# Kernel optimization log

Measured on AMD Instinct MI355X. Metric: run time of the kernel, lower is better.

## Reference

```python
import jax, jax.numpy as jnp
import numpy as np

EPS = 1e-5

def headwise_linear(x, w):
    # x: [B,S,D], w: [NH, DH_out, DH_in] block-diagonal linear per head
    B, S, D = x.shape
    NH, O, DH = w.shape
    xh = x.reshape(B, S, NH, DH)
    return jnp.einsum('bshd,hod->bsho', xh, w).reshape(B, S, NH * O)

def setup_inputs() -> dict:
    key = jax.random.key(0)
    ks = jax.random.split(key, 10)
    B, S, D, NH, K = 8, 4096, 768, 4, 4
    DH = D // NH
    small = (2.0 / (5.0 * D)) ** 0.5  # small_init scale
    return {
        'x': jax.random.normal(ks[0], (B, S, D), jnp.float32),
        'conv_w': jax.random.normal(ks[1], (D, 1, K), jnp.float32) * (1.0 / K ** 0.5),
        'conv_b': jnp.zeros((D,), jnp.float32),
        'w_f': jax.random.normal(ks[2], (NH, DH, DH), jnp.float32) * small,
        'w_i': jax.random.normal(ks[3], (NH, DH, DH), jnp.float32) * small,
        'w_z': jax.random.normal(ks[4], (NH, DH, DH), jnp.float32) * small,
        'w_o': jax.random.normal(ks[5], (NH, DH, DH), jnp.float32) * small,
        'r_kernel': jax.random.normal(ks[6], (NH, DH, 4, DH), jnp.float32) * (1.0 / DH ** 0.5),
        'r_bias': jnp.zeros((4, NH, DH), jnp.float32),
        'gn_weight': jnp.ones((D,), jnp.float32),
    }

def reference(x, conv_w, conv_b, w_f, w_i, w_z, w_o, r_kernel, r_bias, gn_weight):
    B, S, D = x.shape
    NH, DH = r_kernel.shape[0], r_kernel.shape[1]
    K = conv_w.shape[-1]
    # --- causal depthwise conv1d + SiLU ---
    xt = jnp.transpose(x, (0, 2, 1))  # [B,D,S]
    xc = jax.lax.conv_general_dilated(xt, conv_w, (1,), [(K - 1, 0)],
                                      feature_group_count=D)
    x_conv = jax.nn.silu(jnp.transpose(xc + conv_b[None, :, None], (0, 2, 1)))
    # --- headwise gate projections (note: original code feeds fgate->i, igate->f) ---
    gi = headwise_linear(x_conv, w_f)
    gf = headwise_linear(x_conv, w_i)
    gz = headwise_linear(x, w_z)
    go = headwise_linear(x, w_o)
    Wx = jnp.stack([gi, gf, gz, go], axis=2).reshape(B, S, 4, NH, DH)
    Wx = jnp.transpose(Wx, (1, 0, 2, 3, 4))  # [S,B,4,NH,DH]
    # --- sLSTM recurrent scan with exponential gating + stabilizer m ---
    def step(carry, wx_t):
        y, c, n, m = carry  # each [B,NH,DH]
        Ry = jnp.einsum('bhd,hdge->bghe', y, r_kernel)  # [B,4,NH,DH]
        raw = wx_t + Ry + r_bias[None]
        iraw, fraw, zraw, oraw = raw[:, 0], raw[:, 1], raw[:, 2], raw[:, 3]
        logfplusm = m + jax.nn.log_sigmoid(fraw)
        mnew = jnp.maximum(iraw, logfplusm)
        igate = jnp.exp(iraw - mnew)
        fgate = jnp.exp(logfplusm - mnew)
        cnew = fgate * c + igate * jnp.tanh(zraw)
        nnew = fgate * n + igate
        ynew = jax.nn.sigmoid(oraw) * cnew / nnew
        return (ynew, cnew, nnew, mnew), ynew
    init = tuple(jnp.zeros((B, NH, DH), x.dtype) for _ in range(4))
    _, ys = jax.lax.scan(step, init, Wx)  # [S,B,NH,DH]
    y = jnp.transpose(ys, (1, 2, 0, 3))  # [B,NH,S,DH]
    # --- multi-head layer norm (group norm with NH groups over DH) ---
    mean = y.mean(-1, keepdims=True)
    var = y.var(-1, keepdims=True)
    yn = (y - mean) * jax.lax.rsqrt(var + EPS)
    yn = yn * gn_weight.reshape(1, NH, 1, DH)
    return jnp.transpose(yn, (0, 2, 1, 3)).reshape(B, S, NH * DH)
```

## Files before the change

### kernel.cpp

```cpp
#include <hip/hip_runtime.h>
#include <hip/hip_bf16.h>
#include <math.h>

#define B_ 8
#define S_ 4096
#define D_ 768
#define NH_ 4
#define DH_ 192
#define NTOT_ 768

typedef __attribute__((ext_vector_type(8))) short short8;
typedef __attribute__((ext_vector_type(4))) float floatx4;
typedef __attribute__((ext_vector_type(4))) short short4v;
typedef __attribute__((ext_vector_type(4))) unsigned int uint4v;
typedef _Float16 f16;

__device__ __forceinline__ short f2bs(float f) {
  union { float f; unsigned u; } v; v.f = f;
  unsigned r = v.u + 0x7FFFu + ((v.u >> 16) & 1u);
  return (short)(r >> 16);
}
__device__ __forceinline__ float bs2f(unsigned short s) {
  union { unsigned u; float f; } v; v.u = ((unsigned)s) << 16;
  return v.f;
}
__device__ __forceinline__ unsigned packh2(float lo, float hi) {
  union { f16 h[2]; unsigned u; } x;
  x.h[0] = (f16)lo; x.h[1] = (f16)hi;
  return x.u;
}

__device__ __forceinline__ float DOT2(unsigned r, unsigned y, float acc) {
  asm("v_dot2_f32_f16 %0, %1, %2, %0" : "+v"(acc) : "v"(r), "v"(y));
  return acc;
}

template<int CTRL>
__device__ __forceinline__ float qperm(float x) {
  return __int_as_float(__builtin_amdgcn_mov_dpp(__float_as_int(x), CTRL, 0xf, 0xf, true));
}

__global__ __launch_bounds__(256) void wconv_kernel(
    const float* __restrict__ wf, const float* __restrict__ wi,
    const float* __restrict__ wz, const float* __restrict__ wo,
    short* __restrict__ Wbf)
{
  int idx = blockIdx.x * 256 + threadIdx.x;
  int hg = idx / (DH_ * DH_);
  int r  = idx % (DH_ * DH_);
  int h = hg >> 2, g = hg & 3;
  const float* W = (g == 0) ? wf : (g == 1) ? wi : (g == 2) ? wz : wo;
  Wbf[idx] = f2bs(W[(size_t)h * DH_ * DH_ + r]);
}

__global__ __launch_bounds__(256) void conv_silu_kernel(
    const float* __restrict__ x, const float* __restrict__ cw, const float* __restrict__ cb,
    short* __restrict__ xb, short* __restrict__ xcb)
{
  const int b  = blockIdx.x / (S_ / 64);
  const int s0 = (blockIdx.x % (S_ / 64)) * 64;
  const int tid = threadIdx.x;
  float wv[3][4], bias[3], win[3][3];
  for (int j = 0; j < 3; ++j) {
    int d = tid + j * 256;
    for (int k = 0; k < 4; ++k) wv[j][k] = cw[d * 4 + k];
    bias[j] = cb[d];
    for (int p = 0; p < 3; ++p) {
      int s = s0 - 3 + p;
      win[j][p] = (s >= 0) ? x[((size_t)b * S_ + s) * D_ + d] : 0.f;
    }
  }
  for (int i = 0; i < 64; ++i) {
    size_t base = ((size_t)b * S_ + (s0 + i)) * D_;
    for (int j = 0; j < 3; ++j) {
      int d = tid + j * 256;
      float xc = x[base + d];
      float a = bias[j] + win[j][0] * wv[j][0] + win[j][1] * wv[j][1]
                        + win[j][2] * wv[j][2] + xc * wv[j][3];
      float sv = a / (1.f + __expf(-a));
      xb[base + d]  = f2bs(xc);
      xcb[base + d] = f2bs(sv);
      win[j][0] = win[j][1]; win[j][1] = win[j][2]; win[j][2] = xc;
    }
  }
}

__global__ __launch_bounds__(256) void proj_kernel(
    const short* __restrict__ xb, const short* __restrict__ xcb,
    const short* __restrict__ Wbf, const float* __restrict__ rb,
    short* __restrict__ P)
{
  const int hg = blockIdx.y;
  const int h = hg >> 2, g = hg & 3;
  const short* A  = (g < 2) ? xcb : xb;
  const short* Wb = Wbf + (size_t)hg * (DH_ * DH_);
  const int tid = threadIdx.x, w = tid >> 6, l = tid & 63;
  const int l15 = l & 15, lg = l >> 4;
  const int R0 = blockIdx.x * 256 + w * 64;

  float rbv[12];
#pragma unroll
  for (int nt = 0; nt < 12; ++nt)
    rbv[nt] = rb[(g * NH_ + h) * DH_ + l15 + nt * 16];

  for (int mp = 0; mp < 2; ++mp) {
    const int rb0 = R0 + mp * 32;
    floatx4 acc[2][12];
    for (int u = 0; u < 2; ++u)
      for (int nt = 0; nt < 12; ++nt) acc[u][nt] = (floatx4){0.f, 0.f, 0.f, 0.f};
    const short* Ar = A + (size_t)(rb0 + l15) * D_ + h * DH_ + lg * 8;
    const short* Bp = Wb + l15 * DH_ + lg * 8;
    for (int kk = 0; kk < 6; ++kk) {
      short8 a0 = *(const short8*)(Ar + kk * 32);
      short8 a1 = *(const short8*)(Ar + (size_t)16 * D_ + kk * 32);
      for (int nt = 0; nt < 12; ++nt) {
        short8 bf = *(const short8*)(Bp + nt * 16 * DH_ + kk * 32);
        acc[0][nt] = __builtin_amdgcn_mfma_f32_16x16x32_bf16(a0, bf, acc[0][nt], 0, 0, 0);
        acc[1][nt] = __builtin_amdgcn_mfma_f32_16x16x32_bf16(a1, bf, acc[1][nt], 0, 0, 0);
      }
    }
    for (int u = 0; u < 2; ++u) {
      for (int q = 0; q < 4; ++q) {
        int row = rb0 + u * 16 + lg * 4 + q;
        int s = row & (S_ - 1);
        int bb = row >> 12;
        size_t ob = (((size_t)h * B_ + bb) * S_ + s) * NTOT_ + l15 * 4 + g;
        for (int nt = 0; nt < 12; ++nt)
          P[ob + nt * 64] = f2bs(acc[u][nt][q] + rbv[nt]);
      }
    }
  }
}

__global__ __launch_bounds__(768)
void scan_kernel(short* P_, const float* __restrict__ rk)
{
  const int bid = blockIdx.x;
  const int h = bid >> 3;
  const int t0 = threadIdx.x;
  const int e = t0 >> 2, q = t0 & 3;
  const int w = t0 >> 6, l = t0 & 63;
  const int l15 = l & 15, lg = l >> 4;

  __shared__ __align__(16) f16 y_f16[DH_];
  __shared__ __align__(16) unsigned short y_bf[DH_];
  __shared__ __align__(16) float raw_lds[3][DH_];

  const float* Rh = rk + (size_t)h * (DH_ * NTOT_);

  unsigned Ri[24];
#pragma unroll
  for (int j = 0; j < 24; ++j) {
    const int k0 = 48 * q + 2 * j;
    Ri[j] = packh2(Rh[(size_t)k0 * NTOT_ + e], Rh[(size_t)(k0 + 1) * NTOT_ + e]);
  }

  short8 Bf[3][6];
#pragma unroll
  for (int gg = 0; gg < 3; ++gg) {
#pragma unroll
    for (int kk = 0; kk < 6; ++kk) {
      short8 v;
#pragma unroll
      for (int j = 0; j < 8; ++j) {
        const int k = kk * 32 + lg * 8 + j;
        v[j] = f2bs(Rh[(size_t)k * NTOT_ + (gg + 1) * DH_ + w * 16 + l15]);
      }
      Bf[gg][kk] = v;
    }
  }

  if (t0 < DH_) { y_f16[t0] = (f16)0.f; y_bf[t0] = 0; }

  float c = 0.f, nrm = 0.f, m = 0.f;
  short* Pc = P_ + (size_t)bid * S_ * NTOT_;
  short4v wxc = *(const short4v*)(Pc + e * 4);
  __syncthreads();

#pragma unroll 1
  for (int t = 0; t < S_; ++t) {
    short4v wxn = {};
    if (t + 1 < S_) wxn = *(const short4v*)(Pc + (size_t)(t + 1) * NTOT_ + e * 4);

    floatx4 acc0 = (floatx4){0.f,0.f,0.f,0.f};
    floatx4 acc1 = (floatx4){0.f,0.f,0.f,0.f};
    floatx4 acc2 = (floatx4){0.f,0.f,0.f,0.f};
    float a0 = 0.f;
#pragma unroll
    for (int kk = 0; kk < 6; ++kk) {
      short8 A = *(const short8*)((const short*)y_bf + kk * 32 + lg * 8);
      acc0 = __builtin_amdgcn_mfma_f32_16x16x32_bf16(A, Bf[0][kk], acc0, 0, 0, 0);
      acc1 = __builtin_amdgcn_mfma_f32_16x16x32_bf16(A, Bf[1][kk], acc1, 0, 0, 0);
      acc2 = __builtin_amdgcn_mfma_f32_16x16x32_bf16(A, Bf[2][kk], acc2, 0, 0, 0);
      uint4v Y = *(const uint4v*)((const f16*)y_f16 + q * 48 + kk * 8);
      a0 = DOT2(Ri[kk * 4 + 0], Y[0], a0);
      a0 = DOT2(Ri[kk * 4 + 1], Y[1], a0);
      a0 = DOT2(Ri[kk * 4 + 2], Y[2], a0);
      a0 = DOT2(Ri[kk * 4 + 3], Y[3], a0);
    }
    a0 += qperm<0xB1>(a0);  a0 += qperm<0x4E>(a0);
    if (l < 16) {
      raw_lds[0][w * 16 + l] = acc0[0];
      raw_lds[1][w * 16 + l] = acc1[0];
      raw_lds[2][w * 16 + l] = acc2[0];
    }
    __syncthreads();

    float ir  = bs2f((unsigned short)wxc[0]) + a0;
    float fr  = bs2f((unsigned short)wxc[1]) + raw_lds[0][e];
    float zr  = bs2f((unsigned short)wxc[2]) + raw_lds[1][e];
    float orr = bs2f((unsigned short)wxc[3]) + raw_lds[2][e];

    float lsf = fminf(fr, 0.f) - __logf(1.f + __expf(-fabsf(fr)));
    float lfm = m + lsf;
    float mnew = fmaxf(ir, lfm);
    float ig = __expf(ir - mnew);
    float fg = __expf(lfm - mnew);
    float e2z = __expf(2.f * zr);
    float tz = 1.f - 2.f * __builtin_amdgcn_rcpf(e2z + 1.f);
    c   = fg * c + ig * tz;
    nrm = fg * nrm + ig;
    m = mnew;
    float sg = __builtin_amdgcn_rcpf(1.f + __expf(-orr));
    float y = sg * c * __builtin_amdgcn_rcpf(nrm);

    if (q == 0) {
      f16 yh = (f16)y;
      y_f16[e] = yh;
      y_bf[e] = (unsigned short)f2bs(y);
      union { f16 hh; short ss; } uv; uv.hh = yh;
      Pc[(size_t)t * NTOT_ + e] = uv.ss;
    }
    wxc = wxn;
    __syncthreads();
  }
}

__global__ __launch_bounds__(256) void gnorm_kernel(
    const short* __restrict__ yws, const float* __restrict__ gnw,
    float* __restrict__ out)
{
  const int row = blockIdx.x * 4 + (threadIdx.x >> 6);
  const int l = threadIdx.x & 63;
  const int h = row >> 15;
  const int b = (row >> 12) & 7;
  const int s = row & (S_ - 1);
  const short* yr = yws + (size_t)row * NTOT_;
  float v[3];
  float su = 0.f, sq = 0.f;
#pragma unroll
  for (int j = 0; j < 3; ++j) {
    unsigned short u = (unsigned short)yr[l + j * 64];
    union { unsigned short u; f16 h; } cv; cv.u = u;
    v[j] = (float)cv.h;
    su += v[j]; sq += v[j] * v[j];
  }
  for (int off = 32; off; off >>= 1) {
    su += __shfl_xor(su, off);
    sq += __shfl_xor(sq, off);
  }
  float mean = su * (1.f / DH_);
  float var = sq * (1.f / DH_) - mean * mean;
  float rs = rsqrtf(var + 1e-5f);
  float* orow = out + ((size_t)b * S_ + s) * D_ + h * DH_;
#pragma unroll
  for (int j = 0; j < 3; ++j)
    orow[l + j * 64] = (v[j] - mean) * rs * gnw[h * DH_ + l + j * 64];
}

extern "C" void kernel_launch(void* const* d_in, const int* in_sizes, int n_in,
                              void* d_out, int out_size, void* d_ws, size_t ws_size,
                              hipStream_t stream) {
  const float* x   = (const float*)d_in[0];
  const float* cw  = (const float*)d_in[1];
  const float* cb  = (const float*)d_in[2];
  const float* wf  = (const float*)d_in[3];
  const float* wi  = (const float*)d_in[4];
  const float* wz  = (const float*)d_in[5];
  const float* wo  = (const float*)d_in[6];
  const float* rk  = (const float*)d_in[7];
  const float* rb  = (const float*)d_in[8];
  const float* gnw = (const float*)d_in[9];
  float* out = (float*)d_out;

  short* P   = (short*)d_ws;
  short* Wbf = (short*)((char*)d_ws + (size_t)201326592);
  short* xb  = (short*)d_out;
  short* xcb = (short*)((char*)d_out + (size_t)50331648);

  wconv_kernel<<<dim3(2304), 256, 0, stream>>>(wf, wi, wz, wo, Wbf);
  conv_silu_kernel<<<dim3(512), 256, 0, stream>>>(x, cw, cb, xb, xcb);
  proj_kernel<<<dim3(128, 16), 256, 0, stream>>>(xb, xcb, Wbf, rb, P);
  scan_kernel<<<dim3(32), 768, 0, stream>>>(P, rk);
  gnorm_kernel<<<dim3(32768), 256, 0, stream>>>(P, gnw, out);
}
```

Baseline: 5.687 ms.

## Batch all eight sequences per head into one MFMA-based scan block

The recurrent scan now runs one workgroup per head instead of one per head and batch. The eight batch rows fill the MFMA M dimension, so all four gates come from f16 MFMAs and the separate dot2 path for the input gate is gone. Each thread updates two batch states per step, y is double-buffered in LDS, and the gate results move through a per-wave LDS exchange that needs no barrier. That leaves one block barrier per timestep instead of two, at the cost of more serial gate arithmetic per thread, only 4 active workgroups, and f16 instead of bf16 for the recurrent operand.

```diff
diff --git a/kernel.cpp b/kernel.cpp
--- a/kernel.cpp
+++ b/kernel.cpp
@@ -12,8 +12,8 @@
 typedef __attribute__((ext_vector_type(8))) short short8;
 typedef __attribute__((ext_vector_type(4))) float floatx4;
 typedef __attribute__((ext_vector_type(4))) short short4v;
-typedef __attribute__((ext_vector_type(4))) unsigned int uint4v;
 typedef _Float16 f16;
+typedef __attribute__((ext_vector_type(8))) _Float16 h8;
 
 __device__ __forceinline__ short f2bs(float f) {
   union { float f; unsigned u; } v; v.f = f;
@@ -23,21 +23,6 @@
 __device__ __forceinline__ float bs2f(unsigned short s) {
   union { unsigned u; float f; } v; v.u = ((unsigned)s) << 16;
   return v.f;
-}
-__device__ __forceinline__ unsigned packh2(float lo, float hi) {
-  union { f16 h[2]; unsigned u; } x;
-  x.h[0] = (f16)lo; x.h[1] = (f16)hi;
-  return x.u;
-}
-
-__device__ __forceinline__ float DOT2(unsigned r, unsigned y, float acc) {
-  asm("v_dot2_f32_f16 %0, %1, %2, %0" : "+v"(acc) : "v"(r), "v"(y));
-  return acc;
-}
-
-template<int CTRL>
-__device__ __forceinline__ float qperm(float x) {
-  return __int_as_float(__builtin_amdgcn_mov_dpp(__float_as_int(x), CTRL, 0xf, 0xf, true));
 }
 
 __global__ __launch_bounds__(256) void wconv_kernel(
@@ -135,103 +120,123 @@
 __global__ __launch_bounds__(768)
 void scan_kernel(short* P_, const float* __restrict__ rk)
 {
-  const int bid = blockIdx.x;
-  const int h = bid >> 3;
+  const int h  = blockIdx.x;
   const int t0 = threadIdx.x;
-  const int e = t0 >> 2, q = t0 & 3;
-  const int w = t0 >> 6, l = t0 & 63;
+  const int w  = t0 >> 6, l = t0 & 63;
   const int l15 = l & 15, lg = l >> 4;
 
-  __shared__ __align__(16) f16 y_f16[DH_];
-  __shared__ __align__(16) unsigned short y_bf[DH_];
-  __shared__ __align__(16) float raw_lds[3][DH_];
+  __shared__ __align__(16) f16 y_lds[2][16][200];
+  __shared__ __align__(16) float raw_lds[12][8][16][4];
 
   const float* Rh = rk + (size_t)h * (DH_ * NTOT_);
 
-  unsigned Ri[24];
-#pragma unroll
-  for (int j = 0; j < 24; ++j) {
-    const int k0 = 48 * q + 2 * j;
-    Ri[j] = packh2(Rh[(size_t)k0 * NTOT_ + e], Rh[(size_t)(k0 + 1) * NTOT_ + e]);
-  }
-
-  short8 Bf[3][6];
-#pragma unroll
-  for (int gg = 0; gg < 3; ++gg) {
+  h8 Bf[4][6];
+#pragma unroll
+  for (int g = 0; g < 4; ++g) {
 #pragma unroll
     for (int kk = 0; kk < 6; ++kk) {
-      short8 v;
+      h8 v;
 #pragma unroll
       for (int j = 0; j < 8; ++j) {
         const int k = kk * 32 + lg * 8 + j;
-        v[j] = f2bs(Rh[(size_t)k * NTOT_ + (gg + 1) * DH_ + w * 16 + l15]);
+        v[j] = (f16)Rh[(size_t)k * NTOT_ + g * DH_ + w * 16 + l15];
       }
-      Bf[gg][kk] = v;
-    }
-  }
-
-  if (t0 < DH_) { y_f16[t0] = (f16)0.f; y_bf[t0] = 0; }
-
-  float c = 0.f, nrm = 0.f, m = 0.f;
-  short* Pc = P_ + (size_t)bid * S_ * NTOT_;
-  short4v wxc = *(const short4v*)(Pc + e * 4);
+      Bf[g][kk] = v;
+    }
+  }
+
+  for (int idx = t0; idx < 2 * 16 * 200; idx += 768)
+    ((f16*)y_lds)[idx] = (f16)0.f;
+
+  const int e  = w * 16 + l15;
+  const int c0 = lg, c1 = lg + 4;
+  short* Pb0 = P_ + ((size_t)(h * B_ + c0) * S_) * NTOT_;
+  short* Pb1 = P_ + ((size_t)(h * B_ + c1) * S_) * NTOT_;
+
+  float cc0 = 0.f, nn0 = 0.f, mm0 = 0.f;
+  float cc1 = 0.f, nn1 = 0.f, mm1 = 0.f;
+  short4v wxc0 = *(const short4v*)(Pb0 + e * 4);
+  short4v wxc1 = *(const short4v*)(Pb1 + e * 4);
   __syncthreads();
 
 #pragma unroll 1
   for (int t = 0; t < S_; ++t) {
-    short4v wxn = {};
-    if (t + 1 < S_) wxn = *(const short4v*)(Pc + (size_t)(t + 1) * NTOT_ + e * 4);
-
-    floatx4 acc0 = (floatx4){0.f,0.f,0.f,0.f};
-    floatx4 acc1 = (floatx4){0.f,0.f,0.f,0.f};
-    floatx4 acc2 = (floatx4){0.f,0.f,0.f,0.f};
-    float a0 = 0.f;
+    short4v wxn0 = {}, wxn1 = {};
+    if (t + 1 < S_) {
+      wxn0 = *(const short4v*)(Pb0 + (size_t)(t + 1) * NTOT_ + e * 4);
+      wxn1 = *(const short4v*)(Pb1 + (size_t)(t + 1) * NTOT_ + e * 4);
+    }
+    const int cur = t & 1, nxt = cur ^ 1;
+
+    floatx4 a0 = (floatx4){0.f,0.f,0.f,0.f};
+    floatx4 a1 = (floatx4){0.f,0.f,0.f,0.f};
+    floatx4 a2 = (floatx4){0.f,0.f,0.f,0.f};
+    floatx4 a3 = (floatx4){0.f,0.f,0.f,0.f};
 #pragma unroll
     for (int kk = 0; kk < 6; ++kk) {
-      short8 A = *(const short8*)((const short*)y_bf + kk * 32 + lg * 8);
-      acc0 = __builtin_amdgcn_mfma_f32_16x16x32_bf16(A, Bf[0][kk], acc0, 0, 0, 0);
-      acc1 = __builtin_amdgcn_mfma_f32_16x16x32_bf16(A, Bf[1][kk], acc1, 0, 0, 0);
-      acc2 = __builtin_amdgcn_mfma_f32_16x16x32_bf16(A, Bf[2][kk], acc2, 0, 0, 0);
-      uint4v Y = *(const uint4v*)((const f16*)y_f16 + q * 48 + kk * 8);
-      a0 = DOT2(Ri[kk * 4 + 0], Y[0], a0);
-      a0 = DOT2(Ri[kk * 4 + 1], Y[1], a0);
-      a0 = DOT2(Ri[kk * 4 + 2], Y[2], a0);
-      a0 = DOT2(Ri[kk * 4 + 3], Y[3], a0);
-    }
-    a0 += qperm<0xB1>(a0);  a0 += qperm<0x4E>(a0);
-    if (l < 16) {
-      raw_lds[0][w * 16 + l] = acc0[0];
-      raw_lds[1][w * 16 + l] = acc1[0];
-      raw_lds[2][w * 16 + l] = acc2[0];
-    }
-    __syncthreads();
-
-    float ir  = bs2f((unsigned short)wxc[0]) + a0;
-    float fr  = bs2f((unsigned short)wxc[1]) + raw_lds[0][e];
-    float zr  = bs2f((unsigned short)wxc[2]) + raw_lds[1][e];
-    float orr = bs2f((unsigned short)wxc[3]) + raw_lds[2][e];
-
-    float lsf = fminf(fr, 0.f) - __logf(1.f + __expf(-fabsf(fr)));
-    float lfm = m + lsf;
-    float mnew = fmaxf(ir, lfm);
-    float ig = __expf(ir - mnew);
-    float fg = __expf(lfm - mnew);
-    float e2z = __expf(2.f * zr);
-    float tz = 1.f - 2.f * __builtin_amdgcn_rcpf(e2z + 1.f);
-    c   = fg * c + ig * tz;
-    nrm = fg * nrm + ig;
-    m = mnew;
-    float sg = __builtin_amdgcn_rcpf(1.f + __expf(-orr));
-    float y = sg * c * __builtin_amdgcn_rcpf(nrm);
-
-    if (q == 0) {
-      f16 yh = (f16)y;
-      y_f16[e] = yh;
-      y_bf[e] = (unsigned short)f2bs(y);
-      union { f16 hh; short ss; } uv; uv.hh = yh;
-      Pc[(size_t)t * NTOT_ + e] = uv.ss;
-    }
-    wxc = wxn;
+      h8 A = *(const h8*)&y_lds[cur][l15][kk * 32 + lg * 8];
+      a0 = __builtin_amdgcn_mfma_f32_16x16x32_f16(A, Bf[0][kk], a0, 0, 0, 0);
+      a1 = __builtin_amdgcn_mfma_f32_16x16x32_f16(A, Bf[1][kk], a1, 0, 0, 0);
+      a2 = __builtin_amdgcn_mfma_f32_16x16x32_f16(A, Bf[2][kk], a2, 0, 0, 0);
+      a3 = __builtin_amdgcn_mfma_f32_16x16x32_f16(A, Bf[3][kk], a3, 0, 0, 0);
+    }
+    if (l < 32) {
+#pragma unroll
+      for (int j = 0; j < 4; ++j) {
+        floatx4 v = (floatx4){a0[j], a1[j], a2[j], a3[j]};
+        *(floatx4*)&raw_lds[w][lg * 4 + j][l15][0] = v;
+      }
+    }
+    floatx4 r0 = *(const floatx4*)&raw_lds[w][c0][l15][0];
+    floatx4 r1 = *(const floatx4*)&raw_lds[w][c1][l15][0];
+
+    f16 yh0, yh1;
+    {
+      float ir  = bs2f((unsigned short)wxc0[0]) + r0[0];
+      float fr  = bs2f((unsigned short)wxc0[1]) + r0[1];
+      float zr  = bs2f((unsigned short)wxc0[2]) + r0[2];
+      float orr = bs2f((unsigned short)wxc0[3]) + r0[3];
+      float lsf = fminf(fr, 0.f) - __logf(1.f + __expf(-fabsf(fr)));
+      float lfm = mm0 + lsf;
+      float mnew = fmaxf(ir, lfm);
+      float ig = __expf(ir - mnew);
+      float fg = __expf(lfm - mnew);
+      float e2z = __expf(2.f * zr);
+      float tz = 1.f - 2.f * __builtin_amdgcn_rcpf(e2z + 1.f);
+      cc0 = fg * cc0 + ig * tz;
+      nn0 = fg * nn0 + ig;
+      mm0 = mnew;
+      float sg = __builtin_amdgcn_rcpf(1.f + __expf(-orr));
+      yh0 = (f16)(sg * cc0 * __builtin_amdgcn_rcpf(nn0));
+    }
+    {
+      float ir  = bs2f((unsigned short)wxc1[0]) + r1[0];
+      float fr  = bs2f((unsigned short)wxc1[1]) + r1[1];
+      float zr  = bs2f((unsigned short)wxc1[2]) + r1[2];
+      float orr = bs2f((unsigned short)wxc1[3]) + r1[3];
+      float lsf = fminf(fr, 0.f) - __logf(1.f + __expf(-fabsf(fr)));
+      float lfm = mm1 + lsf;
+      float mnew = fmaxf(ir, lfm);
+      float ig = __expf(ir - mnew);
+      float fg = __expf(lfm - mnew);
+      float e2z = __expf(2.f * zr);
+      float tz = 1.f - 2.f * __builtin_amdgcn_rcpf(e2z + 1.f);
+      cc1 = fg * cc1 + ig * tz;
+      nn1 = fg * nn1 + ig;
+      mm1 = mnew;
+      float sg = __builtin_amdgcn_rcpf(1.f + __expf(-orr));
+      yh1 = (f16)(sg * cc1 * __builtin_amdgcn_rcpf(nn1));
+    }
+
+    y_lds[nxt][c0][e] = yh0;
+    y_lds[nxt][c1][e] = yh1;
+    {
+      union { f16 hh; short ss; } u0, u1;
+      u0.hh = yh0; u1.hh = yh1;
+      Pb0[(size_t)t * NTOT_ + e] = u0.ss;
+      Pb1[(size_t)t * NTOT_ + e] = u1.ss;
+    }
+    wxc0 = wxn0; wxc1 = wxn1;
     __syncthreads();
   }
 }
@@ -291,6 +296,6 @@
   wconv_kernel<<<dim3(2304), 256, 0, stream>>>(wf, wi, wz, wo, Wbf);
   conv_silu_kernel<<<dim3(512), 256, 0, stream>>>(x, cw, cb, xb, xcb);
   proj_kernel<<<dim3(128, 16), 256, 0, stream>>>(xb, xcb, Wbf, rb, P);
-  scan_kernel<<<dim3(32), 768, 0, stream>>>(P, rk);
+  scan_kernel<<<dim3(4), 768, 0, stream>>>(P, rk);
   gnorm_kernel<<<dim3(32768), 256, 0, stream>>>(P, gnw, out);
 }
```

After: 5.426 ms. -4.6%, faster.

## Rebalance sLSTM recurrent gates between dot2 VALU and f16 MFMA tiles

Applied to the files above, without the earlier changes.

In the scan kernel, the forget gate's recurrent matvec moves from MFMA to per-thread v_dot2 accumulation, joining the input gate. Only the z and o gates stay on MFMA, with each wave now computing two 16-column tiles. This cuts the MFMA work per wave in the latency-bound per-timestep loop but adds VALU dot work. The MFMA path also switches from bf16 to f16, so a single y buffer feeds both paths and the bf16 conversion and store disappear. The y buffer in LDS is double-buffered by timestep parity.

```diff
diff --git a/kernel.cpp b/kernel.cpp
--- a/kernel.cpp
+++ b/kernel.cpp
@@ -14,6 +14,7 @@
 typedef __attribute__((ext_vector_type(4))) short short4v;
 typedef __attribute__((ext_vector_type(4))) unsigned int uint4v;
 typedef _Float16 f16;
+typedef __attribute__((ext_vector_type(8))) _Float16 h8;
 
 __device__ __forceinline__ short f2bs(float f) {
   union { float f; unsigned u; } v; v.f = f;
@@ -34,7 +35,6 @@
   asm("v_dot2_f32_f16 %0, %1, %2, %0" : "+v"(acc) : "v"(r), "v"(y));
   return acc;
 }
-
 template<int CTRL>
 __device__ __forceinline__ float qperm(float x) {
   return __int_as_float(__builtin_amdgcn_mov_dpp(__float_as_int(x), CTRL, 0xf, 0xf, true));
@@ -142,35 +142,40 @@
   const int w = t0 >> 6, l = t0 & 63;
   const int l15 = l & 15, lg = l >> 4;
 
-  __shared__ __align__(16) f16 y_f16[DH_];
-  __shared__ __align__(16) unsigned short y_bf[DH_];
-  __shared__ __align__(16) float raw_lds[3][DH_];
+  __shared__ __align__(16) f16 y_lds[2][256];
+  __shared__ __align__(16) float raw_lds[2][DH_];
 
   const float* Rh = rk + (size_t)h * (DH_ * NTOT_);
 
-  unsigned Ri[24];
+  unsigned Rr[2][24];
 #pragma unroll
   for (int j = 0; j < 24; ++j) {
     const int k0 = 48 * q + 2 * j;
-    Ri[j] = packh2(Rh[(size_t)k0 * NTOT_ + e], Rh[(size_t)(k0 + 1) * NTOT_ + e]);
-  }
-
-  short8 Bf[3][6];
-#pragma unroll
-  for (int gg = 0; gg < 3; ++gg) {
+    Rr[0][j] = packh2(Rh[(size_t)k0 * NTOT_ + e],
+                      Rh[(size_t)(k0 + 1) * NTOT_ + e]);
+    Rr[1][j] = packh2(Rh[(size_t)k0 * NTOT_ + DH_ + e],
+                      Rh[(size_t)(k0 + 1) * NTOT_ + DH_ + e]);
+  }
+
+  h8 Bf[2][6];
+#pragma unroll
+  for (int tt = 0; tt < 2; ++tt) {
+    const int tile = 2 * w + tt;
+    const int gate = 2 + (tile >= 12);
+    const int ecol = (tile % 12) * 16 + l15;
 #pragma unroll
     for (int kk = 0; kk < 6; ++kk) {
-      short8 v;
+      h8 v;
 #pragma unroll
       for (int j = 0; j < 8; ++j) {
         const int k = kk * 32 + lg * 8 + j;
-        v[j] = f2bs(Rh[(size_t)k * NTOT_ + (gg + 1) * DH_ + w * 16 + l15]);
+        v[j] = (f16)Rh[(size_t)k * NTOT_ + gate * DH_ + ecol];
       }
-      Bf[gg][kk] = v;
-    }
-  }
-
-  if (t0 < DH_) { y_f16[t0] = (f16)0.f; y_bf[t0] = 0; }
+      Bf[tt][kk] = v;
+    }
+  }
+
+  if (t0 < 512) ((f16*)y_lds)[t0] = (f16)0.f;
 
   float c = 0.f, nrm = 0.f, m = 0.f;
   short* Pc = P_ + (size_t)bid * S_ * NTOT_;
@@ -182,34 +187,43 @@
     short4v wxn = {};
     if (t + 1 < S_) wxn = *(const short4v*)(Pc + (size_t)(t + 1) * NTOT_ + e * 4);
 
+    const f16* ycur = y_lds[t & 1];
+
     floatx4 acc0 = (floatx4){0.f,0.f,0.f,0.f};
     floatx4 acc1 = (floatx4){0.f,0.f,0.f,0.f};
-    floatx4 acc2 = (floatx4){0.f,0.f,0.f,0.f};
-    float a0 = 0.f;
 #pragma unroll
     for (int kk = 0; kk < 6; ++kk) {
-      short8 A = *(const short8*)((const short*)y_bf + kk * 32 + lg * 8);
-      acc0 = __builtin_amdgcn_mfma_f32_16x16x32_bf16(A, Bf[0][kk], acc0, 0, 0, 0);
-      acc1 = __builtin_amdgcn_mfma_f32_16x16x32_bf16(A, Bf[1][kk], acc1, 0, 0, 0);
-      acc2 = __builtin_amdgcn_mfma_f32_16x16x32_bf16(A, Bf[2][kk], acc2, 0, 0, 0);
-      uint4v Y = *(const uint4v*)((const f16*)y_f16 + q * 48 + kk * 8);
-      a0 = DOT2(Ri[kk * 4 + 0], Y[0], a0);
-      a0 = DOT2(Ri[kk * 4 + 1], Y[1], a0);
-      a0 = DOT2(Ri[kk * 4 + 2], Y[2], a0);
-      a0 = DOT2(Ri[kk * 4 + 3], Y[3], a0);
+      h8 A = *(const h8*)&ycur[kk * 32 + lg * 8];
+      acc0 = __builtin_amdgcn_mfma_f32_16x16x32_f16(A, Bf[0][kk], acc0, 0, 0, 0);
+      acc1 = __builtin_amdgcn_mfma_f32_16x16x32_f16(A, Bf[1][kk], acc1, 0, 0, 0);
+    }
+
+    const f16* yb = ycur + q * 48;
+    float a0 = 0.f, a1 = 0.f;
+#pragma unroll
+    for (int i = 0; i < 6; ++i) {
+      uint4v Y = *(const uint4v*)(yb + i * 8);
+#pragma unroll
+      for (int u = 0; u < 4; ++u) {
+        const int j = i * 4 + u;
+        a0 = DOT2(Rr[0][j], Y[u], a0);
+        a1 = DOT2(Rr[1][j], Y[u], a1);
+      }
     }
     a0 += qperm<0xB1>(a0);  a0 += qperm<0x4E>(a0);
+    a1 += qperm<0xB1>(a1);  a1 += qperm<0x4E>(a1);
+
     if (l < 16) {
-      raw_lds[0][w * 16 + l] = acc0[0];
-      raw_lds[1][w * 16 + l] = acc1[0];
-      raw_lds[2][w * 16 + l] = acc2[0];
+      const int tile0 = 2 * w, tile1 = 2 * w + 1;
+      raw_lds[tile0 >= 12][(tile0 % 12) * 16 + l15] = acc0[0];
+      raw_lds[tile1 >= 12][(tile1 % 12) * 16 + l15] = acc1[0];
     }
     __syncthreads();
 
     float ir  = bs2f((unsigned short)wxc[0]) + a0;
-    float fr  = bs2f((unsigned short)wxc[1]) + raw_lds[0][e];
-    float zr  = bs2f((unsigned short)wxc[2]) + raw_lds[1][e];
-    float orr = bs2f((unsigned short)wxc[3]) + raw_lds[2][e];
+    float fr  = bs2f((unsigned short)wxc[1]) + a1;
+    float zr  = bs2f((unsigned short)wxc[2]) + raw_lds[0][e];
+    float orr = bs2f((unsigned short)wxc[3]) + raw_lds[1][e];
 
     float lsf = fminf(fr, 0.f) - __logf(1.f + __expf(-fabsf(fr)));
     float lfm = m + lsf;
@@ -224,10 +238,9 @@
     float sg = __builtin_amdgcn_rcpf(1.f + __expf(-orr));
     float y = sg * c * __builtin_amdgcn_rcpf(nrm);
 
+    f16 yh = (f16)y;
     if (q == 0) {
-      f16 yh = (f16)y;
-      y_f16[e] = yh;
-      y_bf[e] = (unsigned short)f2bs(y);
+      y_lds[(t & 1) ^ 1][e] = yh;
       union { f16 hh; short ss; } uv; uv.hh = yh;
       Pc[(size_t)t * NTOT_ + e] = uv.ss;
     }
```

Measured after the change: 5.895 ms. 1.04x slower.
